# Kernel tuning notes

Hardware: AMD Instinct MI355X
Metric: run time of the kernel (lower is better)

Reference implementation:

```python
import jax, jax.numpy as jnp
from jax import lax
import numpy as np

B, T, D, H, C = 64, 512, 256, 1024, 128
ATT_SIG_W = 3.0


def _p(key, shape, scale=0.02):
    return (jax.random.normal(key, shape, dtype=jnp.float32) * scale)


def setup_inputs() -> dict:
    key = jax.random.key(0)
    ks = jax.random.split(key, 16)
    return {
        "x": jax.random.normal(ks[0], (B, T, D), dtype=jnp.float32),
        "i2h_w": _p(ks[1], (D, H)), "i2h_b": jnp.zeros((H,), jnp.float32),
        "h2h_w": _p(ks[2], (H, H)), "h2h_b": jnp.zeros((H,), jnp.float32),
        "fc_w": _p(ks[3], (H, C)), "fc_b": jnp.zeros((C,), jnp.float32),
        "att_wi_fwd": _p(ks[4], (D, 4 * H)), "att_wh_fwd": _p(ks[5], (H, 4 * H)),
        "att_b_fwd": jnp.zeros((4 * H,), jnp.float32),
        "att_wi_bwd": _p(ks[6], (D, 4 * H)), "att_wh_bwd": _p(ks[7], (H, 4 * H)),
        "att_b_bwd": jnp.zeros((4 * H,), jnp.float32),
        "att_fc_w": _p(ks[8], (2 * H, 1)), "att_fc_b": jnp.zeros((1,), jnp.float32),
    }


def _lstm(x_tbd, wi, wh, b):
    # x_tbd: [T,B,D]; precompute input projections as one batched GEMM
    pre = jnp.einsum('tbd,dh->tbh', x_tbd, wi) + b  # [T,B,4H]
    h0 = jnp.zeros((x_tbd.shape[1], wh.shape[0]), x_tbd.dtype)

    def step(carry, p):
        h, c = carry
        g = p + h @ wh
        i, f, gg, o = jnp.split(g, 4, axis=-1)
        c = jax.nn.sigmoid(f) * c + jax.nn.sigmoid(i) * jnp.tanh(gg)
        h = jax.nn.sigmoid(o) * jnp.tanh(c)
        return (h, c), h

    _, hs = lax.scan(step, (h0, h0), pre)
    return hs  # [T,B,H]


def reference(x, i2h_w, i2h_b, h2h_w, h2h_b, fc_w, fc_b,
              att_wi_fwd, att_wh_fwd, att_b_fwd,
              att_wi_bwd, att_wh_bwd, att_b_bwd,
              att_fc_w, att_fc_b):
    xt = jnp.transpose(x, (1, 0, 2))  # [T,B,D] (batch_first transpose)
    # AttentionNet: bidirectional LSTM -> linear -> steep sigmoid gate
    hf = _lstm(xt, att_wi_fwd, att_wh_fwd, att_b_fwd)
    hb = _lstm(xt[::-1], att_wi_bwd, att_wh_bwd, att_b_bwd)[::-1]
    hcat = jnp.concatenate([hf, hb], axis=-1)  # [T,B,2H]
    att_tb = jax.nn.sigmoid(ATT_SIG_W * (hcat @ att_fc_w + att_fc_b))[..., 0]  # [T,B]

    # TAGM recurrence: precompute i2h for all timesteps as one GEMM
    pre_i2h = jnp.einsum('tbd,dh->tbh', xt, i2h_w) + i2h_b  # [T,B,H]
    h0 = jnp.zeros((x.shape[0], h2h_w.shape[0]), x.dtype)

    def step(h, inp):
        p, a = inp  # p:[B,H], a:[B]
        cand = jax.nn.relu(p + h @ h2h_w + h2h_b)
        nh = a[:, None] * cand + (1.0 - a[:, None]) * h
        return nh, None

    h_last, _ = lax.scan(step, h0, (pre_i2h, att_tb))
    out = h_last @ fc_w + fc_b  # [B,C]
    attention = att_tb.T  # [B,T] to match original attention[:, i] layout
    return out, attention
```

## Files before the change

kernel.cpp:

```cpp
#include <hip/hip_runtime.h>
#include <hip/hip_bf16.h>
#include <cstdint>
#include <cstddef>

constexpr int BATCH = 64;
constexpr int SEQ   = 512;
constexpr int DIM   = 256;
constexpr int HID   = 1024;
constexpr int COUT  = 128;
constexpr int KTOT  = DIM + HID;
constexpr int NGATE = 4 * HID;
constexpr float ATT_SIG_W = 3.0f;

using bf16x8 = __attribute__((ext_vector_type(8))) __bf16;
using f32x4  = __attribute__((ext_vector_type(4))) float;
using u32x4  = __attribute__((ext_vector_type(4))) unsigned int;

__device__ __forceinline__ unsigned short f2bf(float f) {
    union { float f; unsigned u; } v; v.f = f;
    unsigned u = v.u;
    u += 0x7fffu + ((u >> 16) & 1u);
    return (unsigned short)(u >> 16);
}

__device__ __forceinline__ float sigm(float x) { return 1.f / (1.f + __expf(-x)); }

__device__ __forceinline__ void store_16B_wt(void* p, u32x4 v) {
    asm volatile("global_store_dwordx4 %0, %1, off sc0 sc1"
                 :: "v"(p), "v"(v) : "memory");
}

#define GLOAD_LDS_COHERENT(gptr, lptr)                                     \
    __builtin_amdgcn_global_load_lds(                                      \
        (const __attribute__((address_space(1))) void*)(gptr),             \
        (__attribute__((address_space(3))) void*)(lptr), 16, 0, 17)

__global__ void transpose_weights(const float* __restrict__ wi,
                                  const float* __restrict__ wh,
                                  unsigned short* __restrict__ out, int N) {
    __shared__ float tile[64][65];
    int ntiles = N >> 6;
    int kt = blockIdx.x / ntiles;
    int nt = blockIdx.x % ntiles;
    int k0 = kt << 6, n0 = nt << 6;
    int a = threadIdx.x & 63, g = threadIdx.x >> 6;
#pragma unroll
    for (int p = 0; p < 16; ++p) {
        int kr = p * 4 + g;
        int k = k0 + kr;
        const float* src = (k < DIM) ? (wi + (size_t)k * N) : (wh + (size_t)(k - DIM) * N);
        tile[kr][a] = src[n0 + a];
    }
    __syncthreads();
#pragma unroll
    for (int p = 0; p < 16; ++p) {
        int nr = p * 4 + g;
        out[(size_t)(n0 + nr) * KTOT + (k0 + a)] = f2bf(tile[a][nr]);
    }
}

__global__ void transpose_x(const float* __restrict__ x, unsigned short* __restrict__ xt) {
    size_t idx = (size_t)blockIdx.x * blockDim.x + threadIdx.x;
    if (idx >= (size_t)SEQ * BATCH * DIM) return;
    int d = idx % DIM;
    size_t r = idx / DIM;
    int b = r % BATCH;
    int t = r / BATCH;
    xt[idx] = f2bf(x[((size_t)b * SEQ + t) * DIM + d]);
}

__global__ void pack_lstm(const unsigned short* __restrict__ WT,
                          unsigned short* __restrict__ out) {
    int cg = blockIdx.x >> 1, kh = blockIdx.x & 1;
    size_t base = (size_t)blockIdx.x * 20480;
#pragma unroll
    for (int j = 0; j < 80; ++j) {
        int idx = threadIdx.x * 80 + j;
        int frag = idx >> 9;
        int rem = idx & 511;
        int lane = rem >> 3, e = rem & 7;
        int nt = frag / 20, ksl = frag % 20;
        int p = nt * 16 + (lane & 15);
        int origcol = (p >> 3) * 1024 + cg * 8 + (p & 7);
        int k = kh * 640 + ksl * 32 + ((lane >> 4) & 3) * 8 + e;
        out[base + idx] = WT[(size_t)origcol * KTOT + k];
    }
}

__global__ void pack_tagm(const unsigned short* __restrict__ WT,
                          unsigned short* __restrict__ out) {
    int cg = blockIdx.x >> 1, kh = blockIdx.x & 1;
    size_t base = (size_t)blockIdx.x * 10240;
#pragma unroll
    for (int j = 0; j < 40; ++j) {
        int idx = threadIdx.x * 40 + j;
        int ksl = idx >> 9;
        int rem = idx & 511;
        int lane = rem >> 3, e = rem & 7;
        int origcol = cg * 16 + (lane & 15);
        int k = kh * 640 + ksl * 32 + ((lane >> 4) & 3) * 8 + e;
        out[base + idx] = WT[(size_t)origcol * KTOT + k];
    }
}

__device__ __forceinline__ void flag_light(unsigned* flags, int base, int cnt,
                                           int myidx, unsigned epoch) {
    asm volatile("s_waitcnt vmcnt(0)" ::: "memory");
    __syncthreads();
    if (threadIdx.x == 0)
        __hip_atomic_store(flags + myidx, epoch, __ATOMIC_RELAXED, __HIP_MEMORY_SCOPE_AGENT);
    if (threadIdx.x < 64) {
        for (;;) {
            bool ok = true;
            for (int j = (int)threadIdx.x; j < cnt; j += 64)
                ok &= (__hip_atomic_load(flags + base + j, __ATOMIC_RELAXED,
                                         __HIP_MEMORY_SCOPE_AGENT) >= epoch);
            if (__all(ok)) break;
            __builtin_amdgcn_s_sleep(1);
        }
    }
    __syncthreads();
}

__device__ __forceinline__ void flag_barrier(unsigned* flags, int base, int cnt,
                                             int myidx, unsigned epoch) {
    __syncthreads();
    if (threadIdx.x == 0) {
        __builtin_amdgcn_fence(__ATOMIC_RELEASE, "agent");
        __hip_atomic_store(flags + myidx, epoch, __ATOMIC_RELAXED, __HIP_MEMORY_SCOPE_AGENT);
    }
    if (threadIdx.x < 64) {
        for (;;) {
            bool ok = true;
            for (int j = (int)threadIdx.x; j < cnt; j += 64)
                ok &= (__hip_atomic_load(flags + base + j, __ATOMIC_RELAXED,
                                         __HIP_MEMORY_SCOPE_AGENT) >= epoch);
            if (__all(ok)) break;
            __builtin_amdgcn_s_sleep(1);
        }
        if (threadIdx.x == 0)
            __builtin_amdgcn_fence(__ATOMIC_ACQUIRE, "agent");
    }
    __syncthreads();
}

__global__ __launch_bounds__(256)
void tagm_fused(const unsigned short* __restrict__ xt,
                const unsigned short* __restrict__ Wfp,
                const unsigned short* __restrict__ Wbp,
                const unsigned short* __restrict__ Wtp,
                const float* __restrict__ bias_f, const float* __restrict__ bias_b,
                const float* __restrict__ attw, const float* __restrict__ att_fc_b,
                const float* __restrict__ i2h_b, const float* __restrict__ h2h_b,
                const float* __restrict__ fc_w, const float* __restrict__ fc_b,
                unsigned short* __restrict__ h_lstm,
                unsigned short* __restrict__ h_tagm,
                float* __restrict__ h_f32,
                float* __restrict__ att_part,
                unsigned* __restrict__ flags,
                float* __restrict__ out) {
    extern __shared__ char smem[];
    char* dumpbase = smem + 65536;
    float* auxf = (float*)(smem + 65536 + 8192);
    unsigned short* hscr = (unsigned short*)(smem + 65536 + 8192 + 4096);

    int tid = threadIdx.x;
    int wave = tid >> 6, lane = tid & 63;
    int bid = blockIdx.x;
    int dir = bid & 1, rh = (bid >> 1) & 1, cg = bid >> 2;
    int nc = wave >> 1, kh = wave & 1;
    int q = lane >> 4, c15 = lane & 15;
    int hc = lane & 7;

    bf16x8 wreg[40];
    {
        const unsigned short* wp = (dir ? Wbp : Wfp)
                                   + (size_t)((cg * 2 + nc) * 2 + kh) * 20480;
#pragma unroll
        for (int f = 0; f < 40; ++f)
            wreg[f] = *(const bf16x8*)(wp + f * 512 + lane * 8);
    }
    int colE = cg * 16 + nc * 8 + hc;
    const float* bias = dir ? bias_b : bias_f;
    float b_ii = bias[colE], b_ff = bias[HID + colE];
    float b_gg = bias[2 * HID + colE], b_oo = bias[3 * HID + colE];
    float attw_l = attw[dir * HID + colE];

    for (int i = tid; i < 512; i += 256) auxf[i] = 0.f;

    flag_light(flags, 256, 256, 256 + bid, 1u);

    for (int t = 0; t < SEQ; ++t) {
        int tx = dir ? (SEQ - 1 - t) : t;
        const unsigned short* xrow = xt + (size_t)tx * BATCH * DIM;
        bf16x8 xa[16];
        if (kh == 0) {
#pragma unroll
            for (int ksl = 0; ksl < 8; ++ksl)
#pragma unroll
                for (int mt = 0; mt < 2; ++mt) {
                    int row = rh * 32 + mt * 16 + c15;
                    xa[ksl * 2 + mt] = *(const bf16x8*)(xrow + row * DIM + ksl * 32 + q * 8);
                }
        }
        if (t > 0) {
            for (;;) {
                bool ok = true;
                if (lane < 16)
                    ok = (__hip_atomic_load(flags + dir * 128 + rh * 64 + wave * 16 + lane,
                                            __ATOMIC_RELAXED,
                                            __HIP_MEMORY_SCOPE_AGENT) >= (unsigned)t);
                if (__all(ok)) break;
                __builtin_amdgcn_s_sleep(1);
            }
        }
        __builtin_amdgcn_sched_barrier(0);
        {
            const char* hsrc = (const char*)h_lstm
                               + (size_t)((dir * 2 + (t & 1)) * 2 + rh) * 65536;
            char* lbase = smem + (size_t)wave * 16384 + (size_t)lane * 16;
#pragma unroll
            for (int i = 0; i < 16; ++i) {
                int s = wave * 1024 + i * 64 + lane;
                GLOAD_LDS_COHERENT(hsrc + (size_t)s * 16, lbase + (size_t)i * 1024);
            }
        }
        __syncthreads();

        f32x4 acc[2][2] = {};
#pragma unroll
        for (int ksl = 0; ksl < 20; ++ksl) {
#pragma unroll
            for (int mt = 0; mt < 2; ++mt) {
                bf16x8 a;
                if (kh == 0 && ksl < 8) {
                    a = xa[ksl * 2 + mt];
                } else {
                    int kcol = kh * 640 + ksl * 32 + q * 8 - 256;
                    a = *(const bf16x8*)(smem + (size_t)(kcol >> 4) * 1024
                                         + (size_t)((kcol >> 3) & 1) * 512
                                         + (size_t)(mt * 16 + c15) * 16);
                }
                acc[mt][0] = __builtin_amdgcn_mfma_f32_16x16x32_bf16(a, wreg[ksl],      acc[mt][0], 0, 0, 0);
                acc[mt][1] = __builtin_amdgcn_mfma_f32_16x16x32_bf16(a, wreg[20 + ksl], acc[mt][1], 0, 0, 0);
            }
        }
        if (kh == 1) {
            float* dp = (float*)(dumpbase + nc * 4096);
#pragma unroll
            for (int mt = 0; mt < 2; ++mt)
#pragma unroll
                for (int nt = 0; nt < 2; ++nt)
                    *(f32x4*)(dp + ((mt * 2 + nt) * 64 + lane) * 4) = acc[mt][nt];
        }
        __syncthreads();
        if (kh == 0) {
            const float* dp = (const float*)(dumpbase + nc * 4096);
            bool low = (lane & 8) == 0;
#pragma unroll
            for (int mt = 0; mt < 2; ++mt) {
                f32x4 g0 = acc[mt][0] + *(const f32x4*)(dp + ((mt * 2 + 0) * 64 + lane) * 4);
                f32x4 g1 = acc[mt][1] + *(const f32x4*)(dp + ((mt * 2 + 1) * 64 + lane) * 4);
                f32x4 av4;
#pragma unroll
                for (int r = 0; r < 4; ++r) {
                    float fo0 = __shfl(g0[r], lane ^ 8);
                    float fo1 = __shfl(g1[r], lane ^ 8);
                    int rl = mt * 16 + q * 4 + r;
                    float si = sigm(g0[r] + b_ii);
                    float sf = sigm(fo0 + b_ff);
                    float tg = tanhf(g1[r] + b_gg);
                    float so = sigm(fo1 + b_oo);
                    float cprev = auxf[rl * 16 + nc * 8 + hc];
                    float cn = sf * cprev + si * tg;
                    float hn = so * tanhf(cn);
                    float av = low ? hn * attw_l : 0.f;
                    av += __shfl_xor(av, 1); av += __shfl_xor(av, 2); av += __shfl_xor(av, 4);
                    av4[r] = av;
                    if (low) {
                        auxf[rl * 16 + nc * 8 + hc] = cn;
                        hscr[nc * 256 + rl * 8 + hc] = f2bf(hn);
                    }
                }
                if (c15 == 0)
                    *(f32x4*)(att_part + (size_t)(bid * 2 + nc) * 16384
                              + (size_t)tx * 32 + (mt * 16 + q * 4)) = av4;
            }
        }
        __syncthreads();
        if (tid < 64) {
            u32x4 v = *(const u32x4*)(hscr + tid * 8);
            store_16B_wt((char*)h_lstm
                         + (size_t)((dir * 2 + ((t + 1) & 1)) * 2 + rh) * 65536
                         + (size_t)(cg * 64 + tid) * 16, v);
            asm volatile("s_waitcnt vmcnt(0)" ::: "memory");
            if (tid == 0)
                __hip_atomic_store(flags + dir * 128 + rh * 64 + cg, (unsigned)(t + 1),
                                   __ATOMIC_RELAXED, __HIP_MEMORY_SCOPE_AGENT);
        }
    }

    flag_barrier(flags, 256, 256, 256 + bid, 2u);
    {
        int i = tid & 127, half = tid >> 7;
        int item = bid * 128 + i;
        int tt = item >> 6, grow = item & 63;
        int rl = grow & 31, rh2 = grow >> 5;
        float s = 0.f;
        const float* p = att_part + (size_t)((half + rh2 * 2) * 2) * 16384
                         + (size_t)tt * 32 + rl;
        for (int cgi = 0; cgi < 64; ++cgi) {
            size_t off = (size_t)cgi * 8 * 16384;
            s += p[off] + p[off + 16384];
        }
        float* red = (float*)dumpbase;
        if (half) red[i] = s;
        __syncthreads();
        if (!half)
            out[BATCH * COUT + grow * SEQ + tt] = sigm(ATT_SIG_W * (s + red[i] + att_fc_b[0]));
    }
    flag_barrier(flags, 256, 256, 256 + bid, 3u);
    if (bid >= 128) return;

    int rhT = bid & 1, cgT = bid >> 1;
    int mhT = (wave >> 1) & 1;
    bf16x8 wt[20];
    {
        const unsigned short* wp = Wtp + (size_t)(cgT * 2 + kh) * 10240;
#pragma unroll
        for (int f = 0; f < 20; ++f)
            wt[f] = *(const bf16x8*)(wp + f * 512 + lane * 8);
    }
    int colT = cgT * 16 + c15;
    float bbT = i2h_b[colT] + h2h_b[colT];
    for (int i = tid; i < 512; i += 256) auxf[i] = 0.f;
    __syncthreads();
    const float* attd = out + BATCH * COUT;

    for (int t = 0; t < SEQ; ++t) {
        const unsigned short* xrow = xt + (size_t)t * BATCH * DIM;
        bf16x8 xa[8];
        if (kh == 0) {
#pragma unroll
            for (int ksl = 0; ksl < 8; ++ksl) {
                int row = rhT * 32 + mhT * 16 + c15;
                xa[ksl] = *(const bf16x8*)(xrow + row * DIM + ksl * 32 + q * 8);
            }
        }
        if (t > 0) {
            for (;;) {
                bool ok = true;
                if (lane < 16)
                    ok = (__hip_atomic_load(flags + 512 + rhT * 64 + wave * 16 + lane,
                                            __ATOMIC_RELAXED,
                                            __HIP_MEMORY_SCOPE_AGENT) >= (unsigned)t);
                if (__all(ok)) break;
                __builtin_amdgcn_s_sleep(1);
            }
        }
        __builtin_amdgcn_sched_barrier(0);
        {
            const char* hsrc = (const char*)h_tagm + (size_t)((t & 1) * 2 + rhT) * 65536;
            char* lbase = smem + (size_t)wave * 16384 + (size_t)lane * 16;
#pragma unroll
            for (int i = 0; i < 16; ++i) {
                int s = wave * 1024 + i * 64 + lane;
                GLOAD_LDS_COHERENT(hsrc + (size_t)s * 16, lbase + (size_t)i * 1024);
            }
        }
        __syncthreads();
        f32x4 acc = {};
#pragma unroll
        for (int ksl = 0; ksl < 20; ++ksl) {
            bf16x8 a;
            if (kh == 0 && ksl < 8) {
                a = xa[ksl];
            } else {
                int kcol = kh * 640 + ksl * 32 + q * 8 - 256;
                a = *(const bf16x8*)(smem + (size_t)(kcol >> 4) * 1024
                                     + (size_t)((kcol >> 3) & 1) * 512
                                     + (size_t)(mhT * 16 + c15) * 16);
            }
            acc = __builtin_amdgcn_mfma_f32_16x16x32_bf16(a, wt[ksl], acc, 0, 0, 0);
        }
        if (kh == 1)
            *(f32x4*)(dumpbase + mhT * 1024 + lane * 16) = acc;
        __syncthreads();
        if (kh == 0) {
            f32x4 g = acc + *(const f32x4*)(dumpbase + mhT * 1024 + lane * 16);
#pragma unroll
            for (int r = 0; r < 4; ++r) {
                int rl = mhT * 16 + q * 4 + r;
                float cand = g[r] + bbT;
                cand = cand > 0.f ? cand : 0.f;
                float a = attd[(rhT * 32 + rl) * SEQ + t];
                float hold = auxf[rl * 16 + c15];
                float hn = a * cand + (1.f - a) * hold;
                auxf[rl * 16 + c15] = hn;
                hscr[(c15 >> 3) * 256 + rl * 8 + (c15 & 7)] = f2bf(hn);
            }
        }
        __syncthreads();
        if (tid < 64) {
            u32x4 v = *(const u32x4*)(hscr + tid * 8);
            store_16B_wt((char*)h_tagm + (size_t)((((t + 1) & 1)) * 2 + rhT) * 65536
                         + (size_t)(cgT * 64 + tid) * 16, v);
            asm volatile("s_waitcnt vmcnt(0)" ::: "memory");
            if (tid == 0)
                __hip_atomic_store(flags + 512 + rhT * 64 + cgT, (unsigned)(t + 1),
                                   __ATOMIC_RELAXED, __HIP_MEMORY_SCOPE_AGENT);
        }
    }

    for (int i = tid; i < 512; i += 256) {
        int rl = i >> 4, cl = i & 15;
        h_f32[(size_t)(rhT * 32 + rl) * HID + cgT * 16 + cl] = auxf[i];
    }
    flag_barrier(flags, 704, 128, 704 + bid, 1u);
    if (bid >= 64) return;

    {
        float* fcp = (float*)dumpbase;
        int c = tid & 127, half = tid >> 7;
        const float* hrow = h_f32 + (size_t)bid * HID;
        float s = 0.f;
        for (int k = half * 512; k < half * 512 + 512; ++k)
            s += hrow[k] * fc_w[(size_t)k * COUT + c];
        fcp[half * 128 + c] = s;
        __syncthreads();
        if (tid < 128)
            out[bid * COUT + tid] = fcp[tid] + fcp[128 + tid] + fc_b[tid];
    }
}

extern "C" void kernel_launch(void* const* d_in, const int* in_sizes, int n_in,
                              void* d_out, int out_size, void* d_ws, size_t ws_size,
                              hipStream_t stream) {
    const float* x          = (const float*)d_in[0];
    const float* i2h_w      = (const float*)d_in[1];
    const float* i2h_b      = (const float*)d_in[2];
    const float* h2h_w      = (const float*)d_in[3];
    const float* h2h_b      = (const float*)d_in[4];
    const float* fc_w       = (const float*)d_in[5];
    const float* fc_b       = (const float*)d_in[6];
    const float* att_wi_fwd = (const float*)d_in[7];
    const float* att_wh_fwd = (const float*)d_in[8];
    const float* att_b_fwd  = (const float*)d_in[9];
    const float* att_wi_bwd = (const float*)d_in[10];
    const float* att_wh_bwd = (const float*)d_in[11];
    const float* att_b_bwd  = (const float*)d_in[12];
    const float* att_fc_w   = (const float*)d_in[13];
    const float* att_fc_b   = (const float*)d_in[14];
    float* out = (float*)d_out;

    char* ws = (char*)d_ws;
    unsigned short* WfT = (unsigned short*)(ws + 0);
    unsigned short* WbT = (unsigned short*)(ws + 10485760);
    unsigned short* WtT = (unsigned short*)(ws + 20971520);
    unsigned short* Wfp = (unsigned short*)(ws + 23592960);
    unsigned short* Wbp = (unsigned short*)(ws + 34078720);
    unsigned short* Wtp = (unsigned short*)(ws + 17829888);
    unsigned short* xtb    = (unsigned short*)(ws + 0);
    unsigned short* h_lstm = (unsigned short*)(ws + 16777216);
    unsigned short* h_tagm = (unsigned short*)(ws + 17301504);
    float*          h_f32  = (float*)(ws + 17563648);
    unsigned*       flags  = (unsigned*)(ws + 17825792);
    float*          att_part = (float*)(ws + 23592960);

    transpose_weights<<<20 * (NGATE / 64), 256, 0, stream>>>(att_wi_fwd, att_wh_fwd, WfT, NGATE);
    transpose_weights<<<20 * (NGATE / 64), 256, 0, stream>>>(att_wi_bwd, att_wh_bwd, WbT, NGATE);
    transpose_weights<<<20 * (HID / 64), 256, 0, stream>>>(i2h_w, h2h_w, WtT, HID);
    pack_lstm<<<256, 256, 0, stream>>>(WfT, Wfp);
    pack_lstm<<<256, 256, 0, stream>>>(WbT, Wbp);
    pack_tagm<<<128, 256, 0, stream>>>(WtT, Wtp);
    transpose_x<<<(SEQ * BATCH * DIM + 255) / 256, 256, 0, stream>>>(x, xtb);
    (void)hipMemsetAsync(ws + 16777216, 0, 17829888 - 16777216, stream);

    static const int SMEM_BYTES = 98304;
    (void)hipFuncSetAttribute(reinterpret_cast<const void*>(tagm_fused),
                              hipFuncAttributeMaxDynamicSharedMemorySize, SMEM_BYTES);
    tagm_fused<<<256, 256, SMEM_BYTES, stream>>>(
        xtb, Wfp, Wbp, Wtp, att_b_fwd, att_b_bwd, att_fc_w, att_fc_b,
        i2h_b, h2h_b, fc_w, fc_b, h_lstm, h_tagm, h_f32, att_part, flags, out);
}
```

Baseline: 6.391 ms.

## Spread TAGM recurrence across all 256 blocks with four-way K split

The TAGM recurrence now runs on all 256 blocks instead of 128. Each block handles 16 batch rows and 16 hidden columns, and each of its four waves owns one quarter of the K dimension, with partial sums reduced through LDS. Weights are repacked into quarter-K fragments to match. The aim is a shorter per-step critical path: fewer MFMAs per wave and half the h tile loaded per block. In exchange, each step needs more cross-block flag synchronisation and an extra LDS reduction.

```diff
diff --git a/kernel.cpp b/kernel.cpp
--- a/kernel.cpp
+++ b/kernel.cpp
@@ -89,16 +89,16 @@
 
 __global__ void pack_tagm(const unsigned short* __restrict__ WT,
                           unsigned short* __restrict__ out) {
-    int cg = blockIdx.x >> 1, kh = blockIdx.x & 1;
-    size_t base = (size_t)blockIdx.x * 10240;
-#pragma unroll
-    for (int j = 0; j < 40; ++j) {
-        int idx = threadIdx.x * 40 + j;
+    int cg = blockIdx.x >> 2, kq = blockIdx.x & 3;
+    size_t base = (size_t)blockIdx.x * 5120;
+#pragma unroll
+    for (int j = 0; j < 20; ++j) {
+        int idx = threadIdx.x * 20 + j;
         int ksl = idx >> 9;
         int rem = idx & 511;
         int lane = rem >> 3, e = rem & 7;
         int origcol = cg * 16 + (lane & 15);
-        int k = kh * 640 + ksl * 32 + ((lane >> 4) & 3) * 8 + e;
+        int k = kq * 320 + ksl * 32 + ((lane >> 4) & 3) * 8 + e;
         out[base + idx] = WT[(size_t)origcol * KTOT + k];
     }
 }
@@ -320,30 +320,29 @@
             out[BATCH * COUT + grow * SEQ + tt] = sigm(ATT_SIG_W * (s + red[i] + att_fc_b[0]));
     }
     flag_barrier(flags, 256, 256, 256 + bid, 3u);
-    if (bid >= 128) return;
-
-    int rhT = bid & 1, cgT = bid >> 1;
-    int mhT = (wave >> 1) & 1;
-    bf16x8 wt[20];
+
+    int rq = bid & 3, cgT = bid >> 2;
+    int kq = wave;
+    bf16x8 wt[10];
     {
-        const unsigned short* wp = Wtp + (size_t)(cgT * 2 + kh) * 10240;
-#pragma unroll
-        for (int f = 0; f < 20; ++f)
+        const unsigned short* wp = Wtp + (size_t)(cgT * 4 + kq) * 5120;
+#pragma unroll
+        for (int f = 0; f < 10; ++f)
             wt[f] = *(const bf16x8*)(wp + f * 512 + lane * 8);
     }
     int colT = cgT * 16 + c15;
     float bbT = i2h_b[colT] + h2h_b[colT];
-    for (int i = tid; i < 512; i += 256) auxf[i] = 0.f;
+    for (int i = tid; i < 256; i += 256) auxf[i] = 0.f;
     __syncthreads();
     const float* attd = out + BATCH * COUT;
 
     for (int t = 0; t < SEQ; ++t) {
-        const unsigned short* xrow = xt + (size_t)t * BATCH * DIM;
         bf16x8 xa[8];
-        if (kh == 0) {
+        if (kq == 0) {
+            const unsigned short* xrow = xt + (size_t)t * BATCH * DIM;
 #pragma unroll
             for (int ksl = 0; ksl < 8; ++ksl) {
-                int row = rhT * 32 + mhT * 16 + c15;
+                int row = rq * 16 + c15;
                 xa[ksl] = *(const bf16x8*)(xrow + row * DIM + ksl * 32 + q * 8);
             }
         }
@@ -351,7 +350,7 @@
             for (;;) {
                 bool ok = true;
                 if (lane < 16)
-                    ok = (__hip_atomic_load(flags + 512 + rhT * 64 + wave * 16 + lane,
+                    ok = (__hip_atomic_load(flags + 512 + rq * 64 + wave * 16 + lane,
                                             __ATOMIC_RELAXED,
                                             __HIP_MEMORY_SCOPE_AGENT) >= (unsigned)t);
                 if (__all(ok)) break;
@@ -360,63 +359,64 @@
         }
         __builtin_amdgcn_sched_barrier(0);
         {
-            const char* hsrc = (const char*)h_tagm + (size_t)((t & 1) * 2 + rhT) * 65536;
-            char* lbase = smem + (size_t)wave * 16384 + (size_t)lane * 16;
-#pragma unroll
-            for (int i = 0; i < 16; ++i) {
-                int s = wave * 1024 + i * 64 + lane;
+            const char* hsrc = (const char*)h_tagm + (size_t)((t & 1) * 4 + rq) * 32768;
+            char* lbase = smem + (size_t)wave * 8192 + (size_t)lane * 16;
+#pragma unroll
+            for (int i = 0; i < 8; ++i) {
+                int s = wave * 512 + i * 64 + lane;
                 GLOAD_LDS_COHERENT(hsrc + (size_t)s * 16, lbase + (size_t)i * 1024);
             }
         }
         __syncthreads();
         f32x4 acc = {};
 #pragma unroll
-        for (int ksl = 0; ksl < 20; ++ksl) {
+        for (int ksl = 0; ksl < 10; ++ksl) {
             bf16x8 a;
-            if (kh == 0 && ksl < 8) {
+            if (kq == 0 && ksl < 8) {
                 a = xa[ksl];
             } else {
-                int kcol = kh * 640 + ksl * 32 + q * 8 - 256;
-                a = *(const bf16x8*)(smem + (size_t)(kcol >> 4) * 1024
-                                     + (size_t)((kcol >> 3) & 1) * 512
-                                     + (size_t)(mhT * 16 + c15) * 16);
+                int kcol = kq * 320 + ksl * 32 + q * 8 - 256;
+                a = *(const bf16x8*)(smem + (size_t)(kcol >> 3) * 256
+                                     + (size_t)c15 * 16);
             }
             acc = __builtin_amdgcn_mfma_f32_16x16x32_bf16(a, wt[ksl], acc, 0, 0, 0);
         }
-        if (kh == 1)
-            *(f32x4*)(dumpbase + mhT * 1024 + lane * 16) = acc;
-        __syncthreads();
-        if (kh == 0) {
-            f32x4 g = acc + *(const f32x4*)(dumpbase + mhT * 1024 + lane * 16);
+        if (kq)
+            *(f32x4*)(dumpbase + (kq - 1) * 1024 + lane * 16) = acc;
+        __syncthreads();
+        if (kq == 0) {
+            f32x4 g = acc + *(const f32x4*)(dumpbase + lane * 16)
+                          + *(const f32x4*)(dumpbase + 1024 + lane * 16)
+                          + *(const f32x4*)(dumpbase + 2048 + lane * 16);
 #pragma unroll
             for (int r = 0; r < 4; ++r) {
-                int rl = mhT * 16 + q * 4 + r;
+                int rl = q * 4 + r;
                 float cand = g[r] + bbT;
                 cand = cand > 0.f ? cand : 0.f;
-                float a = attd[(rhT * 32 + rl) * SEQ + t];
+                float a = attd[(rq * 16 + rl) * SEQ + t];
                 float hold = auxf[rl * 16 + c15];
                 float hn = a * cand + (1.f - a) * hold;
                 auxf[rl * 16 + c15] = hn;
-                hscr[(c15 >> 3) * 256 + rl * 8 + (c15 & 7)] = f2bf(hn);
-            }
-        }
-        __syncthreads();
-        if (tid < 64) {
+                hscr[(c15 >> 3) * 128 + rl * 8 + (c15 & 7)] = f2bf(hn);
+            }
+        }
+        __syncthreads();
+        if (tid < 32) {
             u32x4 v = *(const u32x4*)(hscr + tid * 8);
-            store_16B_wt((char*)h_tagm + (size_t)((((t + 1) & 1)) * 2 + rhT) * 65536
-                         + (size_t)(cgT * 64 + tid) * 16, v);
+            store_16B_wt((char*)h_tagm + (size_t)((((t + 1) & 1)) * 4 + rq) * 32768
+                         + (size_t)(cgT * 32 + tid) * 16, v);
             asm volatile("s_waitcnt vmcnt(0)" ::: "memory");
             if (tid == 0)
-                __hip_atomic_store(flags + 512 + rhT * 64 + cgT, (unsigned)(t + 1),
+                __hip_atomic_store(flags + 512 + rq * 64 + cgT, (unsigned)(t + 1),
                                    __ATOMIC_RELAXED, __HIP_MEMORY_SCOPE_AGENT);
         }
     }
 
-    for (int i = tid; i < 512; i += 256) {
+    for (int i = tid; i < 256; i += 256) {
         int rl = i >> 4, cl = i & 15;
-        h_f32[(size_t)(rhT * 32 + rl) * HID + cgT * 16 + cl] = auxf[i];
-    }
-    flag_barrier(flags, 704, 128, 704 + bid, 1u);
+        h_f32[(size_t)(rq * 16 + rl) * HID + cgT * 16 + cl] = auxf[i];
+    }
+    flag_barrier(flags, 768, 256, 768 + bid, 1u);
     if (bid >= 64) return;
 
     {
@@ -472,7 +472,7 @@
     transpose_weights<<<20 * (HID / 64), 256, 0, stream>>>(i2h_w, h2h_w, WtT, HID);
     pack_lstm<<<256, 256, 0, stream>>>(WfT, Wfp);
     pack_lstm<<<256, 256, 0, stream>>>(WbT, Wbp);
-    pack_tagm<<<128, 256, 0, stream>>>(WtT, Wtp);
+    pack_tagm<<<256, 256, 0, stream>>>(WtT, Wtp);
     transpose_x<<<(SEQ * BATCH * DIM + 255) / 256, 256, 0, stream>>>(x, xtb);
     (void)hipMemsetAsync(ws + 16777216, 0, 17829888 - 16777216, stream);
 
```

Result: faster. 6.219 ms (-2.7%).
